# Kernel tuning notes

Measured on AMD Instinct MI355X. Metric: run time of the kernel, lower is better.

Reference implementation:

```python
import jax, jax.numpy as jnp
import numpy as np

H = 12          # num attention heads
D_HEAD = 64     # head size (768 / 12)
P = 2           # power-law exponent
C = 5.0         # score shift
EPS = 1e-10


def setup_inputs() -> dict:
    key = jax.random.key(0)
    ks = jax.random.split(key, 8)
    B, S, Dm = 32, 512, 768
    scale = 1.0 / np.sqrt(Dm)
    return {
        "hidden_states": jax.random.normal(ks[0], (B, S, Dm), dtype=jnp.float32),
        "attention_mask": jnp.ones((B, 1, 1, S), dtype=jnp.float32),
        "Wq": jax.random.normal(ks[1], (Dm, Dm), dtype=jnp.float32) * scale,
        "bq": jnp.zeros((Dm,), dtype=jnp.float32),
        "Wk": jax.random.normal(ks[2], (Dm, Dm), dtype=jnp.float32) * scale,
        "bk": jnp.zeros((Dm,), dtype=jnp.float32),
        "Wv": jax.random.normal(ks[3], (Dm, Dm), dtype=jnp.float32) * scale,
        "bv": jnp.zeros((Dm,), dtype=jnp.float32),
    }


def _heads(x, B, S):
    # [B, S, H*d] -> [B, H, S, d]
    return x.reshape(B, S, H, D_HEAD).transpose(0, 2, 1, 3)


def reference(hidden_states, attention_mask, Wq, bq, Wk, bk, Wv, bv):
    B, S, Dm = hidden_states.shape
    q = _heads(hidden_states @ Wq + bq, B, S)
    k = _heads(hidden_states @ Wk + bk, B, S)
    v = _heads(hidden_states @ Wv + bv, B, S)

    inv_sqrt_d = 1.0 / (np.sqrt(D_HEAD) + 1e-10)
    scores = jnp.einsum("bhqd,bhkd->bhqk", q, k) * inv_sqrt_d  # [B,H,S,S]

    # Power-law attention (Powerformer, distill=0 branch)
    probs = jnp.power(scores + C, P)
    probs = probs / (jnp.sum(probs, axis=-1, keepdims=True) + EPS)
    probs = probs * attention_mask  # mask multiplied after normalization

    ctx = jnp.einsum("bhqk,bhkd->bhqd", probs, v)  # [B,H,S,d]
    ctx = ctx.transpose(0, 2, 1, 3).reshape(B, S, Dm)
    return ctx
```

## Files before the change

kernel.cpp:

```cpp
#include <hip/hip_runtime.h>

typedef __attribute__((ext_vector_type(8))) _Float16 half8;
typedef __attribute__((ext_vector_type(4))) _Float16 half4;
typedef __attribute__((ext_vector_type(4))) float f32x4;

#define MFMA_K32(a, b, c) __builtin_amdgcn_mfma_f32_16x16x32_f16((a), (b), (c), 0, 0, 0)
#define MFMA_K16(a, b, c) __builtin_amdgcn_mfma_f32_16x16x16f16((a), (b), (c), 0, 0, 0)

__device__ inline void async16(const _Float16* g, _Float16* l) {
    __builtin_amdgcn_global_load_lds(
        (const __attribute__((address_space(1))) void*)g,
        (__attribute__((address_space(3))) void*)l, 16, 0, 0);
}


__global__ __launch_bounds__(256) void xcast(const float* __restrict__ X,
                                             _Float16* __restrict__ Xh)
{
    size_t idx = ((size_t)blockIdx.x * 256 + threadIdx.x) * 8;
    float4 a = *(const float4*)(X + idx);
    float4 c = *(const float4*)(X + idx + 4);
    half8 hv;
    hv[0] = (_Float16)a.x; hv[1] = (_Float16)a.y;
    hv[2] = (_Float16)a.z; hv[3] = (_Float16)a.w;
    hv[4] = (_Float16)c.x; hv[5] = (_Float16)c.y;
    hv[6] = (_Float16)c.z; hv[7] = (_Float16)c.w;
    *(half8*)(Xh + idx) = hv;
}

__global__ __launch_bounds__(256) void wcast_kernel(
    const float* __restrict__ W0, const float* __restrict__ W1,
    const float* __restrict__ W2,
    _Float16* __restrict__ T0, _Float16* __restrict__ T1,
    _Float16* __restrict__ T2)
{
    int z = blockIdx.z;
    const float* W = (z == 0) ? W0 : (z == 1) ? W1 : W2;
    _Float16* T = (z == 0) ? T0 : (z == 1) ? T1 : T2;
    __shared__ float tile[32][33];
    int n0 = blockIdx.x * 32, k0 = blockIdx.y * 32;
    int tx = threadIdx.x & 31, ty = threadIdx.x >> 5;
#pragma unroll
    for (int r = 0; r < 4; ++r)
        tile[ty + 8 * r][tx] = W[(size_t)(k0 + ty + 8 * r) * 768 + n0 + tx];
    __syncthreads();
#pragma unroll
    for (int r = 0; r < 4; ++r)
        T[(size_t)(n0 + ty + 8 * r) * 768 + k0 + tx] =
            (_Float16)tile[tx][ty + 8 * r];
}

__global__ __launch_bounds__(256) void qkv_gemm(
    const _Float16* __restrict__ Xh,
    const _Float16* __restrict__ W0, const _Float16* __restrict__ W1,
    const _Float16* __restrict__ W2,
    const float* __restrict__ b0, const float* __restrict__ b1,
    const float* __restrict__ b2,
    const float* __restrict__ mask,
    _Float16* __restrict__ Qo, _Float16* __restrict__ Ko,
    _Float16* __restrict__ Vo)
{
    int z = blockIdx.y / 6;
    int n0 = (blockIdx.y % 6) * 128;
    int m0 = blockIdx.x * 128;
    const _Float16* Wt = (z == 0) ? W0 : (z == 1) ? W1 : W2;
    const float* bias = (z == 0) ? b0 : (z == 1) ? b1 : b2;

    __shared__ __attribute__((aligned(16))) _Float16 As[128 * 64];
    __shared__ __attribute__((aligned(16))) _Float16 Bs[128 * 64];

    int t = threadIdx.x;
    int wave = t >> 6, lane = t & 63, quad = lane >> 4, l16 = lane & 15;
    int wm = (wave & 1) * 64, wn = (wave >> 1) * 64;

    int srow = t >> 3;
    int sg = (t & 7) ^ (srow & 7);

    const _Float16* gA = Xh + (size_t)(m0 + srow) * 768 + sg * 8;
    const _Float16* gB = Wt + (size_t)(n0 + srow) * 768 + sg * 8;
    _Float16* lA = As + t * 8;
    _Float16* lB = Bs + t * 8;

    f32x4 acc[4][4] = {};

    for (int k0 = 0; k0 < 768; k0 += 64) {
#pragma unroll
        for (int q = 0; q < 4; ++q) {
            async16(gA + (size_t)q * 32 * 768 + k0, lA + q * 2048);
            async16(gB + (size_t)q * 32 * 768 + k0, lB + q * 2048);
        }
        __syncthreads();
#pragma unroll
        for (int ks = 0; ks < 2; ++ks) {
            half8 af[4], bf[4];
#pragma unroll
            for (int i = 0; i < 4; ++i) {
                int row = wm + i * 16 + l16;
                af[i] = *(const half8*)&As[row * 64 +
                                           (((ks << 2) + quad) ^ (row & 7)) * 8];
            }
#pragma unroll
            for (int j = 0; j < 4; ++j) {
                int row = wn + j * 16 + l16;
                bf[j] = *(const half8*)&Bs[row * 64 +
                                           (((ks << 2) + quad) ^ (row & 7)) * 8];
            }
#pragma unroll
            for (int i = 0; i < 4; ++i)
#pragma unroll
                for (int j = 0; j < 4; ++j)
                    acc[i][j] = MFMA_K32(af[i], bf[j], acc[i][j]);
        }
        __syncthreads();
    }

    float mk[4][4];
    if (z == 2) {
#pragma unroll
        for (int i = 0; i < 4; ++i) {
            int mbase = m0 + wm + i * 16 + quad * 4;
            int bb = mbase >> 9, s = mbase & 511;
#pragma unroll
            for (int r = 0; r < 4; ++r)
                mk[i][r] = mask[(size_t)bb * 512 + s + r];
        }
    }
#pragma unroll
    for (int j = 0; j < 4; ++j) {
        int n = n0 + wn + j * 16 + l16;
        float bv = bias[n];
        int hh = n >> 6, d = n & 63;
#pragma unroll
        for (int i = 0; i < 4; ++i) {
            int mbase = m0 + wm + i * 16 + quad * 4;
            int bb = mbase >> 9, s = mbase & 511;
            if (z == 0) {
#pragma unroll
                for (int r = 0; r < 4; ++r) {
                    size_t off = (((size_t)(bb * 12 + hh)) * 512 + s + r) * 64 + d;
                    Qo[off] = (_Float16)((acc[i][j][r] + bv) * 0.125f);
                }
            } else if (z == 1) {
#pragma unroll
                for (int r = 0; r < 4; ++r) {
                    size_t off = (((size_t)(bb * 12 + hh)) * 512 + s + r) * 64 + d;
                    Ko[off] = (_Float16)(acc[i][j][r] + bv);
                }
            } else {
                half4 pk;
#pragma unroll
                for (int r = 0; r < 4; ++r)
                    pk[r] = (_Float16)((acc[i][j][r] + bv) * mk[i][r]);
                size_t off = (((size_t)(bb * 12 + hh)) * 64 + d) * 512 + s;
                *(half4*)&Vo[off] = pk;
            }
        }
    }
}

__global__ __launch_bounds__(256) void attn_kernel(
    const _Float16* __restrict__ Q, const _Float16* __restrict__ K,
    const _Float16* __restrict__ Vt, float* __restrict__ out)
{
    __shared__ __attribute__((aligned(16))) _Float16 Ks[64 * 88];
    __shared__ __attribute__((aligned(16))) _Float16 Vs[64 * 88];

    int t = threadIdx.x;
    int wave = t >> 6, lane = t & 63, quad = lane >> 4, l16 = lane & 15;
    int h = blockIdx.y, b = blockIdx.z;
    size_t bh = (size_t)b * 12 + h;
    const _Float16* Qp = Q + bh * (512 * 64);
    const _Float16* Kp = K + bh * (512 * 64);
    const _Float16* Vp = Vt + bh * (64 * 512);
    int qbase = blockIdx.x * 256 + wave * 64;

    half8 qf[4][2];
#pragma unroll
    for (int i = 0; i < 4; ++i)
#pragma unroll
        for (int ks = 0; ks < 2; ++ks)
            qf[i][ks] = *(const half8*)(Qp + (size_t)(qbase + i * 16 + l16) * 64 +
                                        ks * 32 + quad * 8);

    f32x4 ctx[4][4] = {};
    f32x4 rsum[4] = {};
    const half4 ones = {(_Float16)1.f, (_Float16)1.f, (_Float16)1.f, (_Float16)1.f};

    int srow = t >> 2, spart = (t & 3) * 16;

    for (int kt = 0; kt < 8; ++kt) {
        int k0 = kt * 64;
        const _Float16* kg = Kp + (size_t)(k0 + srow) * 64 + spart;
        half8 ka0 = *(const half8*)kg;
        half8 ka1 = *(const half8*)(kg + 8);
        const _Float16* vg = Vp + (size_t)srow * 512 + k0 + spart;
        half8 va0 = *(const half8*)vg;
        half8 va1 = *(const half8*)(vg + 8);
        __syncthreads();
        *(half8*)&Ks[srow * 88 + spart] = ka0;
        *(half8*)&Ks[srow * 88 + spart + 8] = ka1;
        *(half8*)&Vs[srow * 88 + spart] = va0;
        *(half8*)&Vs[srow * 88 + spart + 8] = va1;
        __syncthreads();

#pragma unroll
        for (int kb = 0; kb < 4; ++kb) {
            half8 kf0 = *(const half8*)&Ks[(kb * 16 + l16) * 88 + quad * 8];
            half8 kf1 = *(const half8*)&Ks[(kb * 16 + l16) * 88 + 32 + quad * 8];
            half4 pA[4];
#pragma unroll
            for (int i = 0; i < 4; ++i) {
                f32x4 sc = {0.f, 0.f, 0.f, 0.f};
                sc = MFMA_K32(kf0, qf[i][0], sc);
                sc = MFMA_K32(kf1, qf[i][1], sc);
                half4 p;
#pragma unroll
                for (int r = 0; r < 4; ++r) {
                    float s = sc[r] + 5.0f;
                    p[r] = (_Float16)(s * s);
                }
                pA[i] = p;
                rsum[i] = MFMA_K16(p, ones, rsum[i]);
            }
#pragma unroll
            for (int n = 0; n < 4; ++n) {
                half4 vf = *(const half4*)&Vs[(n * 16 + l16) * 88 + kb * 16 + quad * 4];
#pragma unroll
                for (int i = 0; i < 4; ++i)
                    ctx[i][n] = MFMA_K16(pA[i], vf, ctx[i][n]);
            }
        }
    }

#pragma unroll
    for (int i = 0; i < 4; ++i) {
        f32x4 inv;
#pragma unroll
        for (int r = 0; r < 4; ++r)
            inv[r] = 1.0f / (rsum[i][r] + 1e-10f);
#pragma unroll
        for (int n = 0; n < 4; ++n)
#pragma unroll
            for (int r = 0; r < 4; ++r) {
                int q = qbase + i * 16 + quad * 4 + r;
                int d = n * 16 + l16;
                out[((size_t)b * 512 + q) * 768 + h * 64 + d] =
                    ctx[i][n][r] * inv[r];
            }
    }
}

extern "C" void kernel_launch(void* const* d_in, const int* in_sizes, int n_in,
                              void* d_out, int out_size, void* d_ws, size_t ws_size,
                              hipStream_t stream)
{
    const float* hs   = (const float*)d_in[0];
    const float* mask = (const float*)d_in[1];
    const float* Wq   = (const float*)d_in[2];
    const float* bq   = (const float*)d_in[3];
    const float* Wk   = (const float*)d_in[4];
    const float* bk   = (const float*)d_in[5];
    const float* Wv   = (const float*)d_in[6];
    const float* bv   = (const float*)d_in[7];
    float* out = (float*)d_out;

    char* ws = (char*)d_ws;
    _Float16* Wtq = (_Float16*)ws;
    _Float16* Wtk = Wtq + 768 * 768;
    _Float16* Wtv = Wtk + 768 * 768;
    _Float16* Qb  = Wtv + 768 * 768;
    _Float16* Kb  = Qb + 16384 * 768;
    _Float16* Vb  = Kb + 16384 * 768;
    _Float16* Xh = (_Float16*)d_out;

    xcast<<<dim3(6144), 256, 0, stream>>>(hs, Xh);
    wcast_kernel<<<dim3(24, 24, 3), 256, 0, stream>>>(Wq, Wk, Wv, Wtq, Wtk, Wtv);
    qkv_gemm<<<dim3(128, 18), 256, 0, stream>>>(Xh, Wtq, Wtk, Wtv,
                                                bq, bk, bv, mask, Qb, Kb, Vb);
    attn_kernel<<<dim3(2, 12, 32), 256, 0, stream>>>(Qb, Kb, Vb, out);
}
```

Baseline: 246.1 us.

## Restructure QKV GEMM into 256x128 tiles with triple-buffered async pipeline

Rewrites the QKV projection GEMM to use 512-thread blocks computing 256x128 tiles. A is triple-buffered and B double-buffered in LDS, with async global-to-LDS loads issued one or two k-steps ahead and synchronised by explicit vmcnt waits and barriers. It also adds a swizzled 1D block index for L2 locality and uses s_setprio around the MFMA bursts. The aim is to hide global load latency that the old load-sync-compute loop exposed. The cost is higher LDS use (about 128KB per block) and hand-tuned wait counts, which are fragile if the issue order changes.

```diff
diff --git a/kernel.cpp b/kernel.cpp
--- a/kernel.cpp
+++ b/kernel.cpp
@@ -50,7 +50,7 @@
             (_Float16)tile[tx][ty + 8 * r];
 }
 
-__global__ __launch_bounds__(256) void qkv_gemm(
+__global__ __launch_bounds__(512, 2) void qkv_gemm(
     const _Float16* __restrict__ Xh,
     const _Float16* __restrict__ W0, const _Float16* __restrict__ W1,
     const _Float16* __restrict__ W2,
@@ -60,97 +60,157 @@
     _Float16* __restrict__ Qo, _Float16* __restrict__ Ko,
     _Float16* __restrict__ Vo)
 {
-    int z = blockIdx.y / 6;
-    int n0 = (blockIdx.y % 6) * 128;
-    int m0 = blockIdx.x * 128;
+    int bid = blockIdx.x;
+    int swz = (bid & 7) * 144 + (bid >> 3);
+    int bx = swz / 18, by = swz % 18;
+    int m0 = bx * 256;
+    int z = by / 6;
+    int n0z = (by % 6) * 128;
+
     const _Float16* Wt = (z == 0) ? W0 : (z == 1) ? W1 : W2;
     const float* bias = (z == 0) ? b0 : (z == 1) ? b1 : b2;
 
-    __shared__ __attribute__((aligned(16))) _Float16 As[128 * 64];
-    __shared__ __attribute__((aligned(16))) _Float16 Bs[128 * 64];
+    __shared__ __attribute__((aligned(16))) _Float16 As[3 * 16384];
+    __shared__ __attribute__((aligned(16))) _Float16 Bs[2 * 8192];
 
     int t = threadIdx.x;
-    int wave = t >> 6, lane = t & 63, quad = lane >> 4, l16 = lane & 15;
-    int wm = (wave & 1) * 64, wn = (wave >> 1) * 64;
-
-    int srow = t >> 3;
-    int sg = (t & 7) ^ (srow & 7);
-
-    const _Float16* gA = Xh + (size_t)(m0 + srow) * 768 + sg * 8;
-    const _Float16* gB = Wt + (size_t)(n0 + srow) * 768 + sg * 8;
-    _Float16* lA = As + t * 8;
-    _Float16* lB = Bs + t * 8;
-
-    f32x4 acc[4][4] = {};
-
-    for (int k0 = 0; k0 < 768; k0 += 64) {
-#pragma unroll
-        for (int q = 0; q < 4; ++q) {
-            async16(gA + (size_t)q * 32 * 768 + k0, lA + q * 2048);
-            async16(gB + (size_t)q * 32 * 768 + k0, lB + q * 2048);
-        }
-        __syncthreads();
-#pragma unroll
-        for (int ks = 0; ks < 2; ++ks) {
-            half8 af[4], bf[4];
-#pragma unroll
-            for (int i = 0; i < 4; ++i) {
-                int row = wm + i * 16 + l16;
-                af[i] = *(const half8*)&As[row * 64 +
-                                           (((ks << 2) + quad) ^ (row & 7)) * 8];
-            }
-#pragma unroll
-            for (int j = 0; j < 4; ++j) {
-                int row = wn + j * 16 + l16;
-                bf[j] = *(const half8*)&Bs[row * 64 +
-                                           (((ks << 2) + quad) ^ (row & 7)) * 8];
-            }
-#pragma unroll
-            for (int i = 0; i < 4; ++i)
-#pragma unroll
-                for (int j = 0; j < 4; ++j)
-                    acc[i][j] = MFMA_K32(af[i], bf[j], acc[i][j]);
-        }
-        __syncthreads();
-    }
-
-    float mk[4][4];
+    int lane = t & 63, quad = lane >> 4, l16 = lane & 15;
+    int wave = t >> 6;
+    int wmi = wave >> 2;
+    int wni = wave & 3;
+
+    int tr = t >> 3;
+    int g = (t & 7) ^ (tr & 7);
+    const _Float16* Asrc = Xh + (size_t)(m0 + tr) * 768 + g * 8;
+    const _Float16* Bsrc = Wt + (size_t)(n0z + tr) * 768 + g * 8;
+    _Float16* Adst = As + t * 8;
+    _Float16* Bdst = Bs + t * 8;
+
+#define STAGE_A_H(bufv, h, k0v) do { \
+        async16(Asrc + (size_t)(2 * (h)) * 49152 + (k0v), \
+                Adst + (bufv) * 16384 + (2 * (h)) * 4096); \
+        async16(Asrc + (size_t)(2 * (h) + 1) * 49152 + (k0v), \
+                Adst + (bufv) * 16384 + (2 * (h) + 1) * 4096); } while (0)
+#define STAGE_B(bufv, k0v) do { \
+        async16(Bsrc + (k0v), Bdst + (bufv) * 8192); \
+        async16(Bsrc + 49152 + (k0v), Bdst + (bufv) * 8192 + 4096); } while (0)
+
+    const _Float16* aR = As + (wmi * 128 + l16) * 64;
+    const _Float16* bR = Bs + (wni * 32 + l16) * 64;
+    int px0 = quad ^ (l16 & 7);
+    int px1 = px0 ^ 4;
+
+    STAGE_A_H(0, 0, 0);
+    STAGE_A_H(0, 1, 0);
+    STAGE_B(0, 0);
+    STAGE_A_H(1, 0, 64);
+    STAGE_A_H(1, 1, 64);
+    STAGE_B(1, 64);
+    asm volatile("s_waitcnt vmcnt(6)" ::: "memory");
+    __builtin_amdgcn_s_barrier();
+
+    f32x4 acc[8][2] = {};
+    int bufR = 0;
+
+    for (int T = 0; T < 12; ++T) {
+        const int k0 = T * 64;
+        const int bB = T & 1;
+        int bS = bufR + 2; if (bS >= 3) bS -= 3;
+        const _Float16* aT = aR + bufR * 16384;
+        const _Float16* bT = bR + bB * 8192;
+        const bool stg = (T < 10);
+
+        half8 bf[2][2], af[4][2];
+
+#pragma unroll
+        for (int ni = 0; ni < 2; ++ni) {
+            bf[ni][0] = *(const half8*)(bT + ni * 1024 + px0 * 8);
+            bf[ni][1] = *(const half8*)(bT + ni * 1024 + px1 * 8);
+        }
+#pragma unroll
+        for (int mi = 0; mi < 4; ++mi) {
+            af[mi][0] = *(const half8*)(aT + mi * 1024 + px0 * 8);
+            af[mi][1] = *(const half8*)(aT + mi * 1024 + px1 * 8);
+        }
+        if (stg) STAGE_A_H(bS, 0, k0 + 128);
+        __builtin_amdgcn_s_barrier();
+        asm volatile("s_waitcnt lgkmcnt(0)" ::: "memory");
+        __builtin_amdgcn_sched_barrier(0);
+        __builtin_amdgcn_s_setprio(1);
+#pragma unroll
+        for (int mi = 0; mi < 4; ++mi)
+#pragma unroll
+            for (int ni = 0; ni < 2; ++ni) {
+                acc[mi][ni] = MFMA_K32(af[mi][0], bf[ni][0], acc[mi][ni]);
+                acc[mi][ni] = MFMA_K32(af[mi][1], bf[ni][1], acc[mi][ni]);
+            }
+        __builtin_amdgcn_s_setprio(0);
+        __builtin_amdgcn_s_barrier();
+
+#pragma unroll
+        for (int mi = 0; mi < 4; ++mi) {
+            af[mi][0] = *(const half8*)(aT + (mi + 4) * 1024 + px0 * 8);
+            af[mi][1] = *(const half8*)(aT + (mi + 4) * 1024 + px1 * 8);
+        }
+        if (stg) { STAGE_A_H(bS, 1, k0 + 128); STAGE_B(bB, k0 + 128); }
+        __builtin_amdgcn_s_barrier();
+        asm volatile("s_waitcnt lgkmcnt(0)" ::: "memory");
+        __builtin_amdgcn_sched_barrier(0);
+        __builtin_amdgcn_s_setprio(1);
+#pragma unroll
+        for (int mi = 0; mi < 4; ++mi)
+#pragma unroll
+            for (int ni = 0; ni < 2; ++ni) {
+                acc[mi + 4][ni] = MFMA_K32(af[mi][0], bf[ni][0], acc[mi + 4][ni]);
+                acc[mi + 4][ni] = MFMA_K32(af[mi][1], bf[ni][1], acc[mi + 4][ni]);
+            }
+        __builtin_amdgcn_s_setprio(0);
+        if (T < 10)       asm volatile("s_waitcnt vmcnt(6)" ::: "memory");
+        else if (T == 10) asm volatile("s_waitcnt vmcnt(0)" ::: "memory");
+        __builtin_amdgcn_s_barrier();
+
+        bufR = (bufR == 2) ? 0 : bufR + 1;
+    }
+#undef STAGE_A_H
+#undef STAGE_B
+
+    float mk[8][4];
     if (z == 2) {
 #pragma unroll
-        for (int i = 0; i < 4; ++i) {
-            int mbase = m0 + wm + i * 16 + quad * 4;
+        for (int mi = 0; mi < 8; ++mi) {
+            int mbase = m0 + wmi * 128 + mi * 16 + quad * 4;
             int bb = mbase >> 9, s = mbase & 511;
 #pragma unroll
             for (int r = 0; r < 4; ++r)
-                mk[i][r] = mask[(size_t)bb * 512 + s + r];
-        }
-    }
-#pragma unroll
-    for (int j = 0; j < 4; ++j) {
-        int n = n0 + wn + j * 16 + l16;
-        float bv = bias[n];
-        int hh = n >> 6, d = n & 63;
-#pragma unroll
-        for (int i = 0; i < 4; ++i) {
-            int mbase = m0 + wm + i * 16 + quad * 4;
+                mk[mi][r] = mask[(size_t)bb * 512 + s + r];
+        }
+    }
+#pragma unroll
+    for (int ni = 0; ni < 2; ++ni) {
+        int nz = n0z + wni * 32 + ni * 16 + l16;
+        float bv = bias[nz];
+        int hh = nz >> 6, d = nz & 63;
+#pragma unroll
+        for (int mi = 0; mi < 8; ++mi) {
+            int mbase = m0 + wmi * 128 + mi * 16 + quad * 4;
             int bb = mbase >> 9, s = mbase & 511;
             if (z == 0) {
 #pragma unroll
                 for (int r = 0; r < 4; ++r) {
                     size_t off = (((size_t)(bb * 12 + hh)) * 512 + s + r) * 64 + d;
-                    Qo[off] = (_Float16)((acc[i][j][r] + bv) * 0.125f);
+                    Qo[off] = (_Float16)((acc[mi][ni][r] + bv) * 0.125f);
                 }
             } else if (z == 1) {
 #pragma unroll
                 for (int r = 0; r < 4; ++r) {
                     size_t off = (((size_t)(bb * 12 + hh)) * 512 + s + r) * 64 + d;
-                    Ko[off] = (_Float16)(acc[i][j][r] + bv);
+                    Ko[off] = (_Float16)(acc[mi][ni][r] + bv);
                 }
             } else {
                 half4 pk;
 #pragma unroll
                 for (int r = 0; r < 4; ++r)
-                    pk[r] = (_Float16)((acc[i][j][r] + bv) * mk[i][r]);
+                    pk[r] = (_Float16)((acc[mi][ni][r] + bv) * mk[mi][r]);
                 size_t off = (((size_t)(bb * 12 + hh)) * 64 + d) * 512 + s;
                 *(half4*)&Vo[off] = pk;
             }
@@ -275,7 +335,7 @@
 
     xcast<<<dim3(6144), 256, 0, stream>>>(hs, Xh);
     wcast_kernel<<<dim3(24, 24, 3), 256, 0, stream>>>(Wq, Wk, Wv, Wtq, Wtk, Wtv);
-    qkv_gemm<<<dim3(128, 18), 256, 0, stream>>>(Xh, Wtq, Wtk, Wtv,
-                                                bq, bk, bv, mask, Qb, Kb, Vb);
+    qkv_gemm<<<dim3(1152), 512, 0, stream>>>(Xh, Wtq, Wtk, Wtv,
+                                             bq, bk, bv, mask, Qb, Kb, Vb);
     attn_kernel<<<dim3(2, 12, 32), 256, 0, stream>>>(Qb, Kb, Vb, out);
 }
```

Measured after the change: 246.6 us. About the same (+0.2%).

## Double-buffer K/V tiles in attention kernel with register prefetch

Applied to the files above, without the earlier changes.

Adds a second LDS buffer for the K and V tiles. The next tile is loaded into registers before the MFMA compute on the current tile and written to the other buffer afterwards, so each iteration needs one barrier instead of two. The score MFMAs for all four row groups are also issued together before the power and row-sum step, which gives the scheduler independent work, and s_setprio raises wave priority during compute. This doubles LDS use and keeps the prefetch registers live through the loop, which may lower occupancy.

```diff
diff --git a/kernel.cpp b/kernel.cpp
--- a/kernel.cpp
+++ b/kernel.cpp
@@ -162,8 +162,8 @@
     const _Float16* __restrict__ Q, const _Float16* __restrict__ K,
     const _Float16* __restrict__ Vt, float* __restrict__ out)
 {
-    __shared__ __attribute__((aligned(16))) _Float16 Ks[64 * 88];
-    __shared__ __attribute__((aligned(16))) _Float16 Vs[64 * 88];
+    __shared__ __attribute__((aligned(16))) _Float16 Ks[2][64 * 88];
+    __shared__ __attribute__((aligned(16))) _Float16 Vs[2][64 * 88];
 
     int t = threadIdx.x;
     int wave = t >> 6, lane = t & 63, quad = lane >> 4, l16 = lane & 15;
@@ -187,49 +187,70 @@
     const half4 ones = {(_Float16)1.f, (_Float16)1.f, (_Float16)1.f, (_Float16)1.f};
 
     int srow = t >> 2, spart = (t & 3) * 16;
+    const _Float16* kgb = Kp + (size_t)srow * 64 + spart;
+    const _Float16* vgb = Vp + (size_t)srow * 512 + spart;
+
+    half8 ka0 = *(const half8*)(kgb);
+    half8 ka1 = *(const half8*)(kgb + 8);
+    half8 va0 = *(const half8*)(vgb);
+    half8 va1 = *(const half8*)(vgb + 8);
+    *(half8*)&Ks[0][srow * 88 + spart] = ka0;
+    *(half8*)&Ks[0][srow * 88 + spart + 8] = ka1;
+    *(half8*)&Vs[0][srow * 88 + spart] = va0;
+    *(half8*)&Vs[0][srow * 88 + spart + 8] = va1;
+    __syncthreads();
 
     for (int kt = 0; kt < 8; ++kt) {
-        int k0 = kt * 64;
-        const _Float16* kg = Kp + (size_t)(k0 + srow) * 64 + spart;
-        half8 ka0 = *(const half8*)kg;
-        half8 ka1 = *(const half8*)(kg + 8);
-        const _Float16* vg = Vp + (size_t)srow * 512 + k0 + spart;
-        half8 va0 = *(const half8*)vg;
-        half8 va1 = *(const half8*)(vg + 8);
-        __syncthreads();
-        *(half8*)&Ks[srow * 88 + spart] = ka0;
-        *(half8*)&Ks[srow * 88 + spart + 8] = ka1;
-        *(half8*)&Vs[srow * 88 + spart] = va0;
-        *(half8*)&Vs[srow * 88 + spart + 8] = va1;
-        __syncthreads();
-
+        int c = kt & 1;
+        if (kt < 7) {
+            size_t ko = (size_t)(kt + 1) * 64;
+            ka0 = *(const half8*)(kgb + ko * 64);
+            ka1 = *(const half8*)(kgb + ko * 64 + 8);
+            va0 = *(const half8*)(vgb + ko);
+            va1 = *(const half8*)(vgb + ko + 8);
+        }
+
+        __builtin_amdgcn_s_setprio(1);
 #pragma unroll
         for (int kb = 0; kb < 4; ++kb) {
-            half8 kf0 = *(const half8*)&Ks[(kb * 16 + l16) * 88 + quad * 8];
-            half8 kf1 = *(const half8*)&Ks[(kb * 16 + l16) * 88 + 32 + quad * 8];
+            half8 kf0 = *(const half8*)&Ks[c][(kb * 16 + l16) * 88 + quad * 8];
+            half8 kf1 = *(const half8*)&Ks[c][(kb * 16 + l16) * 88 + 32 + quad * 8];
+            f32x4 sc[4];
+#pragma unroll
+            for (int i = 0; i < 4; ++i) {
+                f32x4 s0 = {0.f, 0.f, 0.f, 0.f};
+                s0 = MFMA_K32(kf0, qf[i][0], s0);
+                sc[i] = MFMA_K32(kf1, qf[i][1], s0);
+            }
             half4 pA[4];
 #pragma unroll
             for (int i = 0; i < 4; ++i) {
-                f32x4 sc = {0.f, 0.f, 0.f, 0.f};
-                sc = MFMA_K32(kf0, qf[i][0], sc);
-                sc = MFMA_K32(kf1, qf[i][1], sc);
-                half4 p;
 #pragma unroll
                 for (int r = 0; r < 4; ++r) {
-                    float s = sc[r] + 5.0f;
-                    p[r] = (_Float16)(s * s);
+                    float s = sc[i][r] + 5.0f;
+                    pA[i][r] = (_Float16)(s * s);
                 }
-                pA[i] = p;
-                rsum[i] = MFMA_K16(p, ones, rsum[i]);
-            }
+            }
+#pragma unroll
+            for (int i = 0; i < 4; ++i)
+                rsum[i] = MFMA_K16(pA[i], ones, rsum[i]);
 #pragma unroll
             for (int n = 0; n < 4; ++n) {
-                half4 vf = *(const half4*)&Vs[(n * 16 + l16) * 88 + kb * 16 + quad * 4];
+                half4 vf = *(const half4*)&Vs[c][(n * 16 + l16) * 88 + kb * 16 + quad * 4];
 #pragma unroll
                 for (int i = 0; i < 4; ++i)
                     ctx[i][n] = MFMA_K16(pA[i], vf, ctx[i][n]);
             }
         }
+        __builtin_amdgcn_s_setprio(0);
+
+        if (kt < 7) {
+            *(half8*)&Ks[1 - c][srow * 88 + spart] = ka0;
+            *(half8*)&Ks[1 - c][srow * 88 + spart + 8] = ka1;
+            *(half8*)&Vs[1 - c][srow * 88 + spart] = va0;
+            *(half8*)&Vs[1 - c][srow * 88 + spart + 8] = va1;
+        }
+        __syncthreads();
     }
 
 #pragma unroll
```

Result: faster. 240.2 us (-2.4%).
